# Kernel optimization log

Hardware: AMD Instinct MI355X
Metric: run time of the kernel (lower is better)

## Reference

```python
import jax, jax.numpy as jnp
import numpy as np

B, T, F, E, NH, DH = 32, 256, 224, 32, 4, 64
D = F + E            # block input/output width (n_features + embed_dim) = 256
H = NH * DH          # hidden width = 256
NDYADS = 10000

def _ln(x, g, b):
    mu = jnp.mean(x, axis=-1, keepdims=True)
    v = jnp.var(x, axis=-1, keepdims=True)
    return (x - mu) * jax.lax.rsqrt(v + 1e-5) * g + b

def _mlstm_layer(x, ln_g, ln_b, Wq, Wk, Wv, Wi, Wf, bi, bf, Wo, Wp):
    # pre-norm residual mLSTM block (xLSTM paper, eqs. 19-27, stabilized)
    xn = _ln(x, ln_g, ln_b)
    q = (xn @ Wq).reshape(B, T, NH, DH)
    k = (xn @ Wk).reshape(B, T, NH, DH) * (DH ** -0.5)
    v = (xn @ Wv).reshape(B, T, NH, DH)
    o = jax.nn.sigmoid((xn @ Wo).reshape(B, T, NH, DH))
    ip = xn @ Wi + bi   # [B,T,NH] scalar input-gate preact per head
    fp = xn @ Wf + bf   # [B,T,NH] scalar forget-gate preact per head (exp gate)

    def step(carry, inp):
        C, n, m = carry  # C:[B,NH,DH,DH] matrix memory, n:[B,NH,DH], m:[B,NH]
        qt, kt, vt, ot, it, ft = inp
        m_new = jnp.maximum(ft + m, it)
        i_s = jnp.exp(it - m_new)
        f_s = jnp.exp(ft + m - m_new)
        C = f_s[:, :, None, None] * C + i_s[:, :, None, None] * (vt[:, :, :, None] * kt[:, :, None, :])
        n = f_s[:, :, None] * n + i_s[:, :, None] * kt
        num = jnp.einsum('bhde,bhe->bhd', C, qt)
        den = jnp.maximum(jnp.abs(jnp.einsum('bhd,bhd->bh', n, qt)), 1.0)
        h = ot * num / den[:, :, None]
        return (C, n, m_new), h

    init = (jnp.zeros((B, NH, DH, DH), x.dtype),
            jnp.zeros((B, NH, DH), x.dtype),
            jnp.zeros((B, NH), x.dtype))
    xs = tuple(jnp.moveaxis(a, 1, 0) for a in (q, k, v, o, ip, fp))
    _, hs = jax.lax.scan(step, init, xs)
    h = jnp.moveaxis(hs, 0, 1).reshape(B, T, H)
    return x + h @ Wp

def _slstm_layer(x, ln_g, ln_b, Wz, Wi, Wf, Wo, Rz, Ri, Rf, Ro, Wp):
    # pre-norm residual sLSTM block: exp gating, per-head block-diagonal recurrence
    xn = _ln(x, ln_g, ln_b)
    zx = (xn @ Wz).reshape(B, T, NH, DH)
    ix = (xn @ Wi).reshape(B, T, NH, DH)
    fx = (xn @ Wf).reshape(B, T, NH, DH)
    ox = (xn @ Wo).reshape(B, T, NH, DH)
    rmat = lambda h, R: jnp.einsum('bhd,hde->bhe', h, R)

    def step(carry, inp):
        h, c, n, m = carry  # all [B,NH,DH]
        zt, it, ft, ot = inp
        z = jnp.tanh(zt + rmat(h, Rz))
        ip = it + rmat(h, Ri)
        fp = ft + rmat(h, Rf)
        o = jax.nn.sigmoid(ot + rmat(h, Ro))
        m_new = jnp.maximum(fp + m, ip)
        i_s = jnp.exp(ip - m_new)
        f_s = jnp.exp(fp + m - m_new)
        c = f_s * c + i_s * z
        n = f_s * n + i_s
        h = o * c / n
        return (h, c, n, m_new), h

    z0 = jnp.zeros((B, NH, DH), x.dtype)
    xs = tuple(jnp.moveaxis(a, 1, 0) for a in (zx, ix, fx, ox))
    _, hs = jax.lax.scan(step, (z0, z0, z0, z0), xs)
    h = jnp.moveaxis(hs, 0, 1).reshape(B, T, H)
    return x + h @ Wp

def _forward(X, dyad_idx, embed, mp, sp, fc_W, fc_b):
    emb = embed[dyad_idx]                                              # [B,E]
    x = jnp.concatenate([X, jnp.broadcast_to(emb[:, None, :], (B, T, E))], axis=-1)
    # dropout is identity in eval mode
    x = _mlstm_layer(x, *[p[0] for p in mp])   # layer 'm'
    x = _slstm_layer(x, *sp)                   # layer 's'
    x = _mlstm_layer(x, *[p[1] for p in mp])   # layer 'm'
    return x[:, -1, :] @ fc_W + fc_b           # [B, horizon]

def setup_inputs():
    key = jax.random.key(0)
    ks = jax.random.split(key, 24)
    g = lambda i, shape, s=0.02: jax.random.normal(ks[i], shape, jnp.float32) * s
    return {
        'X': jax.random.normal(ks[0], (B, T, F), jnp.float32),
        'dyad_idx': jax.random.randint(ks[1], (B,), 0, NDYADS),
        'embed': g(2, (NDYADS, E), 0.1),
        'm_ln_g': jnp.ones((2, D), jnp.float32),
        'm_ln_b': jnp.zeros((2, D), jnp.float32),
        'm_Wq': g(3, (2, D, H)), 'm_Wk': g(4, (2, D, H)), 'm_Wv': g(5, (2, D, H)),
        'm_Wi': g(6, (2, D, NH)), 'm_Wf': g(7, (2, D, NH)),
        'm_bi': jnp.zeros((2, NH), jnp.float32),
        'm_bf': jnp.ones((2, NH), jnp.float32),
        'm_Wo': g(8, (2, D, H)), 'm_Wp': g(9, (2, H, D)),
        's_ln_g': jnp.ones((D,), jnp.float32),
        's_ln_b': jnp.zeros((D,), jnp.float32),
        's_Wz': g(10, (D, H)), 's_Wi': g(11, (D, H)), 's_Wf': g(12, (D, H)), 's_Wo': g(13, (D, H)),
        's_Rz': g(14, (NH, DH, DH)), 's_Ri': g(15, (NH, DH, DH)),
        's_Rf': g(16, (NH, DH, DH)), 's_Ro': g(17, (NH, DH, DH)),
        's_Wp': g(18, (H, D)),
        'fc_W': g(19, (D, 1)),
        'fc_b': jnp.zeros((1,), jnp.float32),
    }

def reference(X, dyad_idx, embed, m_ln_g, m_ln_b, m_Wq, m_Wk, m_Wv, m_Wi, m_Wf, m_bi, m_bf, m_Wo, m_Wp, s_ln_g, s_ln_b, s_Wz, s_Wi, s_Wf, s_Wo, s_Rz, s_Ri, s_Rf, s_Ro, s_Wp, fc_W, fc_b):
    mp = (m_ln_g, m_ln_b, m_Wq, m_Wk, m_Wv, m_Wi, m_Wf, m_bi, m_bf, m_Wo, m_Wp)
    sp = (s_ln_g, s_ln_b, s_Wz, s_Wi, s_Wf, s_Wo, s_Rz, s_Ri, s_Rf, s_Ro, s_Wp)
    return _forward(X, dyad_idx, embed, mp, sp, fc_W, fc_b)
```

## Files before the change

kernel.cpp:

```cpp
#include <hip/hip_runtime.h>
#include <hip/hip_bf16.h>


#define BT 8192
#define SZ ((size_t)BT * 256)

typedef __attribute__((ext_vector_type(4))) float  f32x4;
typedef __attribute__((ext_vector_type(8))) short  s16x8;

__device__ __forceinline__ float bf2f(unsigned short u) {
    return __uint_as_float(((unsigned int)u) << 16);
}
__device__ __forceinline__ unsigned short f2bf(float f) {
    __hip_bfloat16 h = __float2bfloat16(f);
    return *(unsigned short*)&h;
}
__device__ __forceinline__ float rdlane(float v, int l) {
    return __int_as_float(__builtin_amdgcn_readlane(__float_as_int(v), l));
}

__global__ __launch_bounds__(256) void conv_w(
    const float* mWq, const float* mWk, const float* mWv, const float* mWo,
    const float* mWp, const float* sWz, const float* sWi, const float* sWf,
    const float* sWo, const float* sWp, unsigned short* __restrict__ Wt)
{
    int z = blockIdx.z;
    const float* mp[5] = {mWq, mWk, mWv, mWo, mWp};
    const float* sp[5] = {sWz, sWi, sWf, sWo, sWp};
    const float* src;
    if (z < 5)       src = mp[z];
    else if (z < 10) src = sp[z - 5];
    else             src = mp[z - 10] + 65536;
    int kB = blockIdx.x * 64, nB = blockIdx.y * 64;
    __shared__ unsigned short Ts[64][68];
    int tid = threadIdx.x;
    int r = tid >> 2, c = (tid & 3) * 16;
    #pragma unroll
    for (int j = 0; j < 16; j += 4) {
        float4 wv = *(const float4*)(src + (size_t)(kB + r) * 256 + nB + c + j);
        Ts[r][c + j]     = f2bf(wv.x); Ts[r][c + j + 1] = f2bf(wv.y);
        Ts[r][c + j + 2] = f2bf(wv.z); Ts[r][c + j + 3] = f2bf(wv.w);
    }
    __syncthreads();
    int n = tid >> 2, k0 = (tid & 3) * 16;
    __attribute__((aligned(16))) unsigned short tmp[16];
    #pragma unroll
    for (int j = 0; j < 16; ++j) tmp[j] = Ts[k0 + j][n];
    unsigned short* dst = Wt + (size_t)z * 65536 + (size_t)(nB + n) * 256 + kB + k0;
    *(uint4*)dst       = *(const uint4*)tmp;
    *(uint4*)(dst + 8) = *(const uint4*)(tmp + 8);
}

__global__ __launch_bounds__(256) void build_x(
    const float* __restrict__ X, const int* __restrict__ dyad,
    const float* __restrict__ embed, float* __restrict__ x)
{
    int i = blockIdx.x * 256 + threadIdx.x;
    int d = i & 255, bt = i >> 8, b = bt >> 8;
    x[i] = (d < 224) ? X[bt * 224 + d] : embed[dyad[b] * 32 + (d - 224)];
}

__global__ __launch_bounds__(256) void layernorm(
    const float* __restrict__ x, const float* __restrict__ g,
    const float* __restrict__ b, unsigned short* __restrict__ xn)
{
    int row = blockIdx.x, tid = threadIdx.x;
    float v = x[(size_t)row * 256 + tid];
    float s = v, s2 = v * v;
    #pragma unroll
    for (int o = 32; o; o >>= 1) { s += __shfl_xor(s, o); s2 += __shfl_xor(s2, o); }
    __shared__ float ls[8];
    int wave = tid >> 6, lane = tid & 63;
    if (lane == 0) { ls[wave] = s; ls[4 + wave] = s2; }
    __syncthreads();
    s  = ls[0] + ls[1] + ls[2] + ls[3];
    s2 = ls[4] + ls[5] + ls[6] + ls[7];
    float mu  = s * (1.f / 256.f);
    float var = s2 * (1.f / 256.f) - mu * mu;
    float inv = rsqrtf(var + 1e-5f);
    xn[(size_t)row * 256 + tid] = f2bf((v - mu) * inv * g[tid] + b[tid]);
}

__global__ __launch_bounds__(256) void gemm_mfma_bf16(
    const unsigned short* __restrict__ A, const unsigned short* __restrict__ Wt,
    int slot0, unsigned short* out0, float a0, float a1, float a2, float a3)
{
    __shared__ unsigned short As[64 * 40];
    __shared__ unsigned short Bs[64 * 40];
    int tid = threadIdx.x, bz = blockIdx.z;
    const unsigned short* W = Wt + (size_t)(slot0 + bz) * 65536;
    unsigned short* out = out0 + (size_t)bz * SZ;
    float alpha = bz == 0 ? a0 : bz == 1 ? a1 : bz == 2 ? a2 : a3;
    int rowBase = blockIdx.x * 64, colBase = blockIdx.y * 64;
    int srow = tid >> 2, scol = (tid & 3) * 8;
    const unsigned short* Ap = A + (size_t)(rowBase + srow) * 256 + scol;
    const unsigned short* Wp = W + (size_t)(colBase + srow) * 256 + scol;
    unsigned short* Asw = As + srow * 40 + scol;
    unsigned short* Bsw = Bs + srow * 40 + scol;
    int w = tid >> 6, lane = tid & 63, quad = lane >> 4, l15 = lane & 15;
    const unsigned short* Ar  = As + (w * 16 + l15) * 40 + quad * 8;
    const unsigned short* Br0 = Bs + l15 * 40 + quad * 8;
    f32x4 acc[4];
    #pragma unroll
    for (int c = 0; c < 4; ++c) acc[c] = (f32x4){0.f, 0.f, 0.f, 0.f};
    for (int k0 = 0; k0 < 256; k0 += 32) {
        uint4 av = *(const uint4*)(Ap + k0);
        uint4 bv = *(const uint4*)(Wp + k0);
        __syncthreads();
        *(uint4*)Asw = av;
        *(uint4*)Bsw = bv;
        __syncthreads();
        s16x8 af = *(const s16x8*)Ar;
        #pragma unroll
        for (int c = 0; c < 4; ++c) {
            s16x8 bf = *(const s16x8*)(Br0 + c * 16 * 40);
            acc[c] = __builtin_amdgcn_mfma_f32_16x16x32_bf16(af, bf, acc[c], 0, 0, 0);
        }
    }
    #pragma unroll
    for (int c = 0; c < 4; ++c) {
        int col  = colBase + c * 16 + l15;
        int row0 = rowBase + w * 16 + quad * 4;
        #pragma unroll
        for (int i2 = 0; i2 < 4; ++i2)
            out[(size_t)(row0 + i2) * 256 + col] = f2bf(alpha * acc[c][i2]);
    }
}

__global__ __launch_bounds__(256) void gemm_mfma_f32(
    const unsigned short* __restrict__ A, const unsigned short* __restrict__ Wt,
    int slot, float* __restrict__ out, const float* __restrict__ Res)
{
    __shared__ unsigned short As[64 * 40];
    __shared__ unsigned short Bs[64 * 40];
    int tid = threadIdx.x;
    const unsigned short* W = Wt + (size_t)slot * 65536;
    int rowBase = blockIdx.x * 64, colBase = blockIdx.y * 64;
    int srow = tid >> 2, scol = (tid & 3) * 8;
    const unsigned short* Ap = A + (size_t)(rowBase + srow) * 256 + scol;
    const unsigned short* Wp = W + (size_t)(colBase + srow) * 256 + scol;
    unsigned short* Asw = As + srow * 40 + scol;
    unsigned short* Bsw = Bs + srow * 40 + scol;
    int w = tid >> 6, lane = tid & 63, quad = lane >> 4, l15 = lane & 15;
    const unsigned short* Ar  = As + (w * 16 + l15) * 40 + quad * 8;
    const unsigned short* Br0 = Bs + l15 * 40 + quad * 8;
    f32x4 acc[4];
    #pragma unroll
    for (int c = 0; c < 4; ++c) acc[c] = (f32x4){0.f, 0.f, 0.f, 0.f};
    for (int k0 = 0; k0 < 256; k0 += 32) {
        uint4 av = *(const uint4*)(Ap + k0);
        uint4 bv = *(const uint4*)(Wp + k0);
        __syncthreads();
        *(uint4*)Asw = av;
        *(uint4*)Bsw = bv;
        __syncthreads();
        s16x8 af = *(const s16x8*)Ar;
        #pragma unroll
        for (int c = 0; c < 4; ++c) {
            s16x8 bf = *(const s16x8*)(Br0 + c * 16 * 40);
            acc[c] = __builtin_amdgcn_mfma_f32_16x16x32_bf16(af, bf, acc[c], 0, 0, 0);
        }
    }
    #pragma unroll
    for (int c = 0; c < 4; ++c) {
        int col  = colBase + c * 16 + l15;
        int row0 = rowBase + w * 16 + quad * 4;
        #pragma unroll
        for (int i2 = 0; i2 < 4; ++i2) {
            size_t idx = (size_t)(row0 + i2) * 256 + col;
            out[idx] = acc[c][i2] + Res[idx];
        }
    }
}

__global__ __launch_bounds__(256) void gate_gemm(
    const unsigned short* __restrict__ xn,
    const float* __restrict__ Wi, const float* __restrict__ Wf,
    const float* __restrict__ bi, const float* __restrict__ bf_,
    float* __restrict__ gi, float* __restrict__ gf)
{
    int tid = threadIdx.x;
    int hh = tid & 3;
    int row = blockIdx.x * 64 + (tid >> 2);
    float ai = bi[hh], af = bf_[hh];
    const unsigned short* xr = xn + (size_t)row * 256;
    for (int k2 = 0; k2 < 256; ++k2) {
        float xv = bf2f(xr[k2]);
        ai += xv * Wi[k2 * 4 + hh];
        af += xv * Wf[k2 * 4 + hh];
    }
    gi[row * 4 + hh] = ai;
    gf[row * 4 + hh] = af;
}

__global__ __launch_bounds__(256) void scan_am(
    const float* __restrict__ gi, const float* __restrict__ gf,
    float* __restrict__ a_arr, float* __restrict__ M_arr)
{
    int bh = blockIdx.x, b = bh >> 2, h = bh & 3;
    int t = threadIdx.x;
    float fp = gf[(b * 256 + t) * 4 + h];
    float ip = gi[(b * 256 + t) * 4 + h];
    __shared__ float buf[256];
    buf[t] = fp;
    __syncthreads();
    #pragma unroll
    for (int o = 1; o < 256; o <<= 1) {
        float add = (t >= o) ? buf[t - o] : 0.f;
        __syncthreads();
        buf[t] += add;
        __syncthreads();
    }
    float F = buf[t];
    float a = ip - F;
    __syncthreads();
    buf[t] = a;
    __syncthreads();
    #pragma unroll
    for (int o = 1; o < 256; o <<= 1) {
        float mx = (t >= o) ? buf[t - o] : -3.4e38f;
        __syncthreads();
        buf[t] = fmaxf(buf[t], mx);
        __syncthreads();
    }
    a_arr[bh * 256 + t] = a;
    M_arr[bh * 256 + t] = fmaxf(buf[t], 0.f);
}

__global__ __launch_bounds__(256) void mlstm_attn(
    const unsigned short* __restrict__ qb, const unsigned short* __restrict__ kb,
    const unsigned short* __restrict__ vb, const unsigned short* __restrict__ ob,
    const float* __restrict__ a_arr, const float* __restrict__ M_arr,
    unsigned short* __restrict__ hout)
{
    int bh = blockIdx.x, rt = blockIdx.y;
    int b = bh >> 2, h = bh & 3;
    int tid = threadIdx.x, w = tid >> 6, lane = tid & 63;
    int quad = lane >> 4, l15 = lane & 15;
    __shared__ unsigned short Qs[64][72];
    __shared__ unsigned short Ks[64][72];
    __shared__ unsigned short Vt[64][72];
    __shared__ unsigned short Ps[4][16][72];
    __shared__ float a_s[64], M_s[64];
    int sr = tid >> 2, sc = (tid & 3) * 16;
    size_t qoff = (size_t)(b * 256 + rt * 64 + sr) * 256 + h * 64 + sc;
    *(uint4*)&Qs[sr][sc]     = *(const uint4*)(qb + qoff);
    *(uint4*)&Qs[sr][sc + 8] = *(const uint4*)(qb + qoff + 8);
    if (tid < 64) M_s[tid] = M_arr[bh * 256 + rt * 64 + tid];
    f32x4 accN[4];
    #pragma unroll
    for (int c = 0; c < 4; ++c) accN[c] = (f32x4){0.f, 0.f, 0.f, 0.f};
    f32x4 den = (f32x4){0.f, 0.f, 0.f, 0.f};
    int rowT = w * 16 + quad * 4;
    for (int ct = 0; ct <= rt; ++ct) {
        size_t koff = (size_t)(b * 256 + ct * 64 + sr) * 256 + h * 64 + sc;
        uint4 kv0 = *(const uint4*)(kb + koff);
        uint4 kv1 = *(const uint4*)(kb + koff + 8);
        uint4 vv0 = *(const uint4*)(vb + koff);
        uint4 vv1 = *(const uint4*)(vb + koff + 8);
        *(uint4*)&Ks[sr][sc]     = kv0;
        *(uint4*)&Ks[sr][sc + 8] = kv1;
        __attribute__((aligned(16))) unsigned short vt[16];
        *(uint4*)vt = vv0; *(uint4*)(vt + 8) = vv1;
        #pragma unroll
        for (int jj = 0; jj < 16; ++jj) Vt[sc + jj][sr] = vt[jj];
        if (tid < 64) a_s[tid] = a_arr[bh * 256 + ct * 64 + tid];
        __syncthreads();
        f32x4 S[4];
        #pragma unroll
        for (int c = 0; c < 4; ++c) S[c] = (f32x4){0.f, 0.f, 0.f, 0.f};
        #pragma unroll
        for (int ks = 0; ks < 2; ++ks) {
            s16x8 af = *(const s16x8*)&Qs[w * 16 + l15][quad * 8 + ks * 32];
            #pragma unroll
            for (int c = 0; c < 4; ++c) {
                s16x8 bfr = *(const s16x8*)&Ks[c * 16 + l15][quad * 8 + ks * 32];
                S[c] = __builtin_amdgcn_mfma_f32_16x16x32_bf16(af, bfr, S[c], 0, 0, 0);
            }
        }
        bool dg = (ct == rt);
        #pragma unroll
        for (int c = 0; c < 4; ++c) {
            int col = c * 16 + l15;
            #pragma unroll
            for (int i2 = 0; i2 < 4; ++i2) {
                int row = rowT + i2;
                float p = S[c][i2] * __expf(a_s[col] - M_s[row]);
                if (dg && col > row) p = 0.f;
                S[c][i2] = p;
                den[i2] += p;
            }
        }
        #pragma unroll
        for (int c = 0; c < 4; ++c)
            #pragma unroll
            for (int i2 = 0; i2 < 4; ++i2)
                Ps[w][quad * 4 + i2][c * 16 + l15] = f2bf(S[c][i2]);
        __syncthreads();
        #pragma unroll
        for (int ks = 0; ks < 2; ++ks) {
            s16x8 af = *(const s16x8*)&Ps[w][l15][quad * 8 + ks * 32];
            #pragma unroll
            for (int c = 0; c < 4; ++c) {
                s16x8 bfr = *(const s16x8*)&Vt[c * 16 + l15][quad * 8 + ks * 32];
                accN[c] = __builtin_amdgcn_mfma_f32_16x16x32_bf16(af, bfr, accN[c], 0, 0, 0);
            }
        }
        __syncthreads();
    }
    #pragma unroll
    for (int ofs = 1; ofs < 16; ofs <<= 1) {
        den[0] += __shfl_xor(den[0], ofs);
        den[1] += __shfl_xor(den[1], ofs);
        den[2] += __shfl_xor(den[2], ofs);
        den[3] += __shfl_xor(den[3], ofs);
    }
    #pragma unroll
    for (int c = 0; c < 4; ++c) {
        int d = c * 16 + l15;
        #pragma unroll
        for (int i2 = 0; i2 < 4; ++i2) {
            size_t idx = (size_t)(b * 256 + rt * 64 + rowT + i2) * 256 + h * 64 + d;
            float ov = bf2f(ob[idx]);
            float sg = 1.f / (1.f + __expf(-ov));
            float dn = fmaxf(fabsf(den[i2]), 1.f);
            hout[idx] = f2bf(sg * accN[c][i2] / dn);
        }
    }
}

__global__ __launch_bounds__(256) void slstm_scan(
    const unsigned short* __restrict__ zx, const unsigned short* __restrict__ ix,
    const unsigned short* __restrict__ fx, const unsigned short* __restrict__ ox,
    const float* __restrict__ Rz, const float* __restrict__ Ri,
    const float* __restrict__ Rf, const float* __restrict__ Ro,
    unsigned short* __restrict__ hout)
{
    int bh = blockIdx.x, b = bh >> 2, h = bh & 3;
    int tid = threadIdx.x, w = tid >> 6, e = tid & 63;
    const float* R = (w == 0 ? Rz : w == 1 ? Ri : w == 2 ? Rf : Ro) + h * 4096;
    float r[64];
    #pragma unroll
    for (int d = 0; d < 64; ++d) r[d] = R[d * 64 + e];
    const unsigned short* xin = (w == 0 ? zx : w == 1 ? ix : w == 2 ? fx : ox);
    __shared__ float gl[2][4][64];
    float c = 0.f, n = 0.f, m = 0.f, hv = 0.f;
    size_t base = (size_t)b * 65536 + h * 64 + e;
    float gx = bf2f(xin[base]);
    for (int t = 0; t < 256; ++t) {
        float a0 = 0.f, a1 = 0.f, a2 = 0.f, a3 = 0.f;
        #pragma unroll
        for (int d = 0; d < 64; d += 4) {
            a0 += rdlane(hv, d)     * r[d];
            a1 += rdlane(hv, d + 1) * r[d + 1];
            a2 += rdlane(hv, d + 2) * r[d + 2];
            a3 += rdlane(hv, d + 3) * r[d + 3];
        }
        gl[t & 1][w][e] = gx + ((a0 + a1) + (a2 + a3));
        int tn = (t + 1 < 256) ? t + 1 : t;
        float gxn = bf2f(xin[base + (size_t)tn * 256]);
        __syncthreads();
        float zp = gl[t & 1][0][e], ip = gl[t & 1][1][e];
        float fp = gl[t & 1][2][e], op = gl[t & 1][3][e];
        float ez = __expf(2.f * zp);
        float z  = 1.f - 2.f / (ez + 1.f);
        float mn = fmaxf(fp + m, ip);
        float i_s = __expf(ip - mn), f_s = __expf(fp + m - mn);
        m = mn;
        c = f_s * c + i_s * z;
        n = f_s * n + i_s;
        hv = (1.f / (1.f + __expf(-op))) * c / n;
        if (w == 0) hout[base + (size_t)t * 256] = f2bf(hv);
        gx = gxn;
    }
}

__global__ __launch_bounds__(64) void fc_kernel(
    const float* __restrict__ x, const float* __restrict__ fcW,
    const float* __restrict__ fcb, float* __restrict__ out)
{
    int b = blockIdx.x, lane = threadIdx.x;
    const float* xr = x + ((size_t)b * 256 + 255) * 256;
    float s = 0.f;
    #pragma unroll
    for (int j = 0; j < 4; ++j) { int d = j * 64 + lane; s += xr[d] * fcW[d]; }
    #pragma unroll
    for (int ofs = 32; ofs; ofs >>= 1) s += __shfl_xor(s, ofs);
    if (lane == 0) out[b] = s + fcb[0];
}

extern "C" void kernel_launch(void* const* d_in, const int* in_sizes, int n_in,
                              void* d_out, int out_size, void* d_ws, size_t ws_size,
                              hipStream_t stream)
{
    const float* X      = (const float*)d_in[0];
    const int*   dyad   = (const int*)d_in[1];
    const float* embed  = (const float*)d_in[2];
    const float* m_ln_g = (const float*)d_in[3];
    const float* m_ln_b = (const float*)d_in[4];
    const float* m_Wq   = (const float*)d_in[5];
    const float* m_Wk   = (const float*)d_in[6];
    const float* m_Wv   = (const float*)d_in[7];
    const float* m_Wi   = (const float*)d_in[8];
    const float* m_Wf   = (const float*)d_in[9];
    const float* m_bi   = (const float*)d_in[10];
    const float* m_bf   = (const float*)d_in[11];
    const float* m_Wo   = (const float*)d_in[12];
    const float* m_Wp   = (const float*)d_in[13];
    const float* s_ln_g = (const float*)d_in[14];
    const float* s_ln_b = (const float*)d_in[15];
    const float* s_Wz   = (const float*)d_in[16];
    const float* s_Wi   = (const float*)d_in[17];
    const float* s_Wf   = (const float*)d_in[18];
    const float* s_Wo   = (const float*)d_in[19];
    const float* s_Rz   = (const float*)d_in[20];
    const float* s_Ri   = (const float*)d_in[21];
    const float* s_Rf   = (const float*)d_in[22];
    const float* s_Ro   = (const float*)d_in[23];
    const float* s_Wp   = (const float*)d_in[24];
    const float* fcW    = (const float*)d_in[25];
    const float* fcb    = (const float*)d_in[26];

    float* ws = (float*)d_ws;
    float* x     = ws;
    float* gi    = x + SZ;
    float* gf    = gi + (size_t)BT * 4;
    float* a_arr = gf + (size_t)BT * 4;
    float* M_arr = a_arr + 32768;
    unsigned short* xn  = (unsigned short*)(M_arr + 32768);
    unsigned short* hb  = xn + SZ;
    unsigned short* g0u = hb + SZ;
    unsigned short* g1u = g0u + SZ;
    unsigned short* g2u = g1u + SZ;
    unsigned short* g3u = g2u + SZ;
    unsigned short* Wt  = g3u + SZ;

    conv_w<<<dim3(4, 4, 15), 256, 0, stream>>>(m_Wq, m_Wk, m_Wv, m_Wo, m_Wp,
                                               s_Wz, s_Wi, s_Wf, s_Wo, s_Wp, Wt);
    build_x<<<8192, 256, 0, stream>>>(X, dyad, embed, x);

    dim3 gg(128, 4);

    auto mlstm = [&](int L) {
        layernorm<<<BT, 256, 0, stream>>>(x, m_ln_g + L * 256, m_ln_b + L * 256, xn);
        gemm_mfma_bf16<<<dim3(128, 4, 4), 256, 0, stream>>>(
            xn, Wt, L * 10, g0u, 1.f, 0.125f, 1.f, 1.f);
        gate_gemm<<<BT / 64, 256, 0, stream>>>(xn, m_Wi + L * 1024, m_Wf + L * 1024,
                                               m_bi + L * 4, m_bf + L * 4, gi, gf);
        scan_am<<<128, 256, 0, stream>>>(gi, gf, a_arr, M_arr);
        mlstm_attn<<<gg, 256, 0, stream>>>(g0u, g1u, g2u, g3u, a_arr, M_arr, hb);
        gemm_mfma_f32<<<dim3(128, 4, 1), 256, 0, stream>>>(hb, Wt, L * 10 + 4, x, x);
    };

    mlstm(0);

    layernorm<<<BT, 256, 0, stream>>>(x, s_ln_g, s_ln_b, xn);
    gemm_mfma_bf16<<<dim3(128, 4, 4), 256, 0, stream>>>(
        xn, Wt, 5, g0u, 1.f, 1.f, 1.f, 1.f);
    slstm_scan<<<128, 256, 0, stream>>>(g0u, g1u, g2u, g3u,
                                        s_Rz, s_Ri, s_Rf, s_Ro, hb);
    gemm_mfma_f32<<<dim3(128, 4, 1), 256, 0, stream>>>(hb, Wt, 9, x, x);

    mlstm(1);

    fc_kernel<<<32, 64, 0, stream>>>(x, fcW, fcb, (float*)d_out);
}
```

Before: 370.7 us.

## Run sLSTM recurrence in a single wave using packed fp16 FMAs

The sLSTM scan kernel shrinks from four waves (one per gate) that synchronise through shared memory every timestep to a single 64-lane wave that computes all four gate recurrences itself. The recurrent weights are held as packed half2 registers, and the hidden-state broadcast uses readlane on a packed pair of values. This removes the per-step __syncthreads and LDS round trip and halves the number of FMA instructions. The cost is fp16 accumulation in the recurrent matvec, which risks precision drift over 256 steps, and each wave now does four times the gate work.

```diff
diff --git a/kernel.cpp b/kernel.cpp
--- a/kernel.cpp
+++ b/kernel.cpp
@@ -1,5 +1,6 @@
 #include <hip/hip_runtime.h>
 #include <hip/hip_bf16.h>
+#include <hip/hip_fp16.h>
 
 
 #define BT 8192
@@ -14,9 +15,6 @@
 __device__ __forceinline__ unsigned short f2bf(float f) {
     __hip_bfloat16 h = __float2bfloat16(f);
     return *(unsigned short*)&h;
-}
-__device__ __forceinline__ float rdlane(float v, int l) {
-    return __int_as_float(__builtin_amdgcn_readlane(__float_as_int(v), l));
 }
 
 __global__ __launch_bounds__(256) void conv_w(
@@ -329,7 +327,7 @@
     }
 }
 
-__global__ __launch_bounds__(256) void slstm_scan(
+__global__ __launch_bounds__(64) void slstm_scan(
     const unsigned short* __restrict__ zx, const unsigned short* __restrict__ ix,
     const unsigned short* __restrict__ fx, const unsigned short* __restrict__ ox,
     const float* __restrict__ Rz, const float* __restrict__ Ri,
@@ -337,41 +335,61 @@
     unsigned short* __restrict__ hout)
 {
     int bh = blockIdx.x, b = bh >> 2, h = bh & 3;
-    int tid = threadIdx.x, w = tid >> 6, e = tid & 63;
-    const float* R = (w == 0 ? Rz : w == 1 ? Ri : w == 2 ? Rf : Ro) + h * 4096;
-    float r[64];
-    #pragma unroll
-    for (int d = 0; d < 64; ++d) r[d] = R[d * 64 + e];
-    const unsigned short* xin = (w == 0 ? zx : w == 1 ? ix : w == 2 ? fx : ox);
-    __shared__ float gl[2][4][64];
+    int e = threadIdx.x;
+    const float* R0 = Rz + h * 4096;
+    const float* R1 = Ri + h * 4096;
+    const float* R2 = Rf + h * 4096;
+    const float* R3 = Ro + h * 4096;
+    __half2 rp0[32], rp1[32], rp2[32], rp3[32];
+    #pragma unroll
+    for (int j = 0; j < 32; ++j) {
+        int o0 = (2 * j) * 64 + e, o1 = (2 * j + 1) * 64 + e;
+        rp0[j] = __floats2half2_rn(R0[o0], R0[o1]);
+        rp1[j] = __floats2half2_rn(R1[o0], R1[o1]);
+        rp2[j] = __floats2half2_rn(R2[o0], R2[o1]);
+        rp3[j] = __floats2half2_rn(R3[o0], R3[o1]);
+    }
     float c = 0.f, n = 0.f, m = 0.f, hv = 0.f;
-    size_t base = (size_t)b * 65536 + h * 64 + e;
-    float gx = bf2f(xin[base]);
+    size_t base = (size_t)(b * 256) * 256 + (size_t)(h * 64 + e);
+    float zv = bf2f(zx[base]), iv = bf2f(ix[base]);
+    float fv = bf2f(fx[base]), ov = bf2f(ox[base]);
+    const __half2 Z2 = __float2half2_rn(0.f);
     for (int t = 0; t < 256; ++t) {
-        float a0 = 0.f, a1 = 0.f, a2 = 0.f, a3 = 0.f;
-        #pragma unroll
-        for (int d = 0; d < 64; d += 4) {
-            a0 += rdlane(hv, d)     * r[d];
-            a1 += rdlane(hv, d + 1) * r[d + 1];
-            a2 += rdlane(hv, d + 2) * r[d + 2];
-            a3 += rdlane(hv, d + 3) * r[d + 3];
-        }
-        gl[t & 1][w][e] = gx + ((a0 + a1) + (a2 + a3));
+        float hn = __shfl_xor(hv, 1);
+        __half2 hp = __floats2half2_rn(hv, hn);
+        union { __half2 h2; unsigned int u; } cv; cv.h2 = hp;
+        unsigned int hbits = cv.u;
+        __half2 A00 = Z2, A01 = Z2, A10 = Z2, A11 = Z2;
+        __half2 A20 = Z2, A21 = Z2, A30 = Z2, A31 = Z2;
+        #pragma unroll
+        for (int j = 0; j < 32; j += 2) {
+            union { unsigned int u; __half2 h2; } c0, c1;
+            c0.u = (unsigned int)__builtin_amdgcn_readlane((int)hbits, 2 * j);
+            c1.u = (unsigned int)__builtin_amdgcn_readlane((int)hbits, 2 * j + 2);
+            A00 = __hfma2(c0.h2, rp0[j], A00);  A01 = __hfma2(c1.h2, rp0[j + 1], A01);
+            A10 = __hfma2(c0.h2, rp1[j], A10);  A11 = __hfma2(c1.h2, rp1[j + 1], A11);
+            A20 = __hfma2(c0.h2, rp2[j], A20);  A21 = __hfma2(c1.h2, rp2[j + 1], A21);
+            A30 = __hfma2(c0.h2, rp3[j], A30);  A31 = __hfma2(c1.h2, rp3[j + 1], A31);
+        }
+        __half2 Az = __hadd2(A00, A01), Ai = __hadd2(A10, A11);
+        __half2 Af = __hadd2(A20, A21), Ao = __hadd2(A30, A31);
+        float zp  = zv + __low2float(Az) + __high2float(Az);
+        float ip2 = iv + __low2float(Ai) + __high2float(Ai);
+        float fp  = fv + __low2float(Af) + __high2float(Af);
+        float op  = ov + __low2float(Ao) + __high2float(Ao);
         int tn = (t + 1 < 256) ? t + 1 : t;
-        float gxn = bf2f(xin[base + (size_t)tn * 256]);
-        __syncthreads();
-        float zp = gl[t & 1][0][e], ip = gl[t & 1][1][e];
-        float fp = gl[t & 1][2][e], op = gl[t & 1][3][e];
+        size_t nb = base + (size_t)tn * 256;
+        zv = bf2f(zx[nb]); iv = bf2f(ix[nb]);
+        fv = bf2f(fx[nb]); ov = bf2f(ox[nb]);
         float ez = __expf(2.f * zp);
         float z  = 1.f - 2.f / (ez + 1.f);
-        float mn = fmaxf(fp + m, ip);
-        float i_s = __expf(ip - mn), f_s = __expf(fp + m - mn);
+        float mn = fmaxf(fp + m, ip2);
+        float i_s = __expf(ip2 - mn), f_s = __expf(fp + m - mn);
         m = mn;
         c = f_s * c + i_s * z;
         n = f_s * n + i_s;
-        hv = (1.f / (1.f + __expf(-op))) * c / n;
-        if (w == 0) hout[base + (size_t)t * 256] = f2bf(hv);
-        gx = gxn;
+        hv = c / (n * (1.f + __expf(-op)));
+        hout[base + (size_t)t * 256] = f2bf(hv);
     }
 }
 
@@ -457,8 +475,8 @@
     layernorm<<<BT, 256, 0, stream>>>(x, s_ln_g, s_ln_b, xn);
     gemm_mfma_bf16<<<dim3(128, 4, 4), 256, 0, stream>>>(
         xn, Wt, 5, g0u, 1.f, 1.f, 1.f, 1.f);
-    slstm_scan<<<128, 256, 0, stream>>>(g0u, g1u, g2u, g3u,
-                                        s_Rz, s_Ri, s_Rf, s_Ro, hb);
+    slstm_scan<<<128, 64, 0, stream>>>(g0u, g1u, g2u, g3u,
+                                       s_Rz, s_Ri, s_Rf, s_Ro, hb);
     gemm_mfma_f32<<<dim3(128, 4, 1), 256, 0, stream>>>(hb, Wt, 9, x, x);
 
     mlstm(1);
```

Measured after the change: 412.6 us. +11.3%, slower.

## Batch sLSTM recurrence across all batches per head using MFMA

Applied to the files above, without the earlier changes.

The sLSTM scan moves from one block per (batch, head) to one block per head that handles all 32 batch rows. Each timestep's recurrent matvec becomes a bf16 MFMA GEMM over [32x64]x[64x64] for the four gates, with h exchanged through double-buffered shared memory. This removes the serial readlane dot products but drops parallelism to only 4 blocks. It also rounds h and the R matrices to bf16 inside the recurrence, which can introduce numerical drift.

```diff
diff --git a/kernel.cpp b/kernel.cpp
--- a/kernel.cpp
+++ b/kernel.cpp
@@ -1,5 +1,6 @@
 #include <hip/hip_runtime.h>
 #include <hip/hip_bf16.h>
+#include <hip/hip_fp16.h>
 
 
 #define BT 8192
@@ -14,9 +15,6 @@
 __device__ __forceinline__ unsigned short f2bf(float f) {
     __hip_bfloat16 h = __float2bfloat16(f);
     return *(unsigned short*)&h;
-}
-__device__ __forceinline__ float rdlane(float v, int l) {
-    return __int_as_float(__builtin_amdgcn_readlane(__float_as_int(v), l));
 }
 
 __global__ __launch_bounds__(256) void conv_w(
@@ -329,49 +327,105 @@
     }
 }
 
-__global__ __launch_bounds__(256) void slstm_scan(
+__global__ __launch_bounds__(512) void slstm_scan(
     const unsigned short* __restrict__ zx, const unsigned short* __restrict__ ix,
     const unsigned short* __restrict__ fx, const unsigned short* __restrict__ ox,
     const float* __restrict__ Rz, const float* __restrict__ Ri,
     const float* __restrict__ Rf, const float* __restrict__ Ro,
     unsigned short* __restrict__ hout)
 {
-    int bh = blockIdx.x, b = bh >> 2, h = bh & 3;
-    int tid = threadIdx.x, w = tid >> 6, e = tid & 63;
-    const float* R = (w == 0 ? Rz : w == 1 ? Ri : w == 2 ? Rf : Ro) + h * 4096;
-    float r[64];
-    #pragma unroll
-    for (int d = 0; d < 64; ++d) r[d] = R[d * 64 + e];
-    const unsigned short* xin = (w == 0 ? zx : w == 1 ? ix : w == 2 ? fx : ox);
-    __shared__ float gl[2][4][64];
-    float c = 0.f, n = 0.f, m = 0.f, hv = 0.f;
-    size_t base = (size_t)b * 65536 + h * 64 + e;
-    float gx = bf2f(xin[base]);
+    int hd = blockIdx.x;
+    int tid = threadIdx.x, w = tid >> 6, lane = tid & 63;
+    int mt = w >> 2, nt = w & 3, quad = lane >> 4, l15 = lane & 15;
+    __shared__ unsigned short hbuf[2][32][72];
+
+    const float* Rg0 = Rz + hd * 4096;
+    const float* Rg1 = Ri + hd * 4096;
+    const float* Rg2 = Rf + hd * 4096;
+    const float* Rg3 = Ro + hd * 4096;
+    int ecol = nt * 16 + l15;
+    s16x8 bfrag[4][2];
+    #pragma unroll
+    for (int ks = 0; ks < 2; ++ks) {
+        int dbase = ks * 32 + quad * 8;
+        #pragma unroll
+        for (int j = 0; j < 8; ++j) {
+            int off = (dbase + j) * 64 + ecol;
+            bfrag[0][ks][j] = (short)f2bf(Rg0[off]);
+            bfrag[1][ks][j] = (short)f2bf(Rg1[off]);
+            bfrag[2][ks][j] = (short)f2bf(Rg2[off]);
+            bfrag[3][ks][j] = (short)f2bf(Rg3[off]);
+        }
+    }
+    for (int i = tid; i < 2 * 32 * 72; i += 512)
+        ((unsigned short*)hbuf)[i] = 0;
+
+    int b0 = mt * 16 + quad * 4;
+    const unsigned short* xg0 = zx; const unsigned short* xg1 = ix;
+    const unsigned short* xg2 = fx; const unsigned short* xg3 = ox;
+    size_t xbase[4];
+    #pragma unroll
+    for (int r = 0; r < 4; ++r)
+        xbase[r] = (size_t)(b0 + r) * 65536 + hd * 64 + ecol;
+
+    unsigned short xc[4][4];
+    #pragma unroll
+    for (int r = 0; r < 4; ++r) {
+        xc[0][r] = xg0[xbase[r]]; xc[1][r] = xg1[xbase[r]];
+        xc[2][r] = xg2[xbase[r]]; xc[3][r] = xg3[xbase[r]];
+    }
+    float cst[4] = {0.f, 0.f, 0.f, 0.f};
+    float nst[4] = {0.f, 0.f, 0.f, 0.f};
+    float mst[4] = {0.f, 0.f, 0.f, 0.f};
+    __syncthreads();
+
+    int cur = 0;
+    int arow = mt * 16 + l15;
     for (int t = 0; t < 256; ++t) {
-        float a0 = 0.f, a1 = 0.f, a2 = 0.f, a3 = 0.f;
-        #pragma unroll
-        for (int d = 0; d < 64; d += 4) {
-            a0 += rdlane(hv, d)     * r[d];
-            a1 += rdlane(hv, d + 1) * r[d + 1];
-            a2 += rdlane(hv, d + 2) * r[d + 2];
-            a3 += rdlane(hv, d + 3) * r[d + 3];
-        }
-        gl[t & 1][w][e] = gx + ((a0 + a1) + (a2 + a3));
-        int tn = (t + 1 < 256) ? t + 1 : t;
-        float gxn = bf2f(xin[base + (size_t)tn * 256]);
-        __syncthreads();
-        float zp = gl[t & 1][0][e], ip = gl[t & 1][1][e];
-        float fp = gl[t & 1][2][e], op = gl[t & 1][3][e];
-        float ez = __expf(2.f * zp);
-        float z  = 1.f - 2.f / (ez + 1.f);
-        float mn = fmaxf(fp + m, ip);
-        float i_s = __expf(ip - mn), f_s = __expf(fp + m - mn);
-        m = mn;
-        c = f_s * c + i_s * z;
-        n = f_s * n + i_s;
-        hv = (1.f / (1.f + __expf(-op))) * c / n;
-        if (w == 0) hout[base + (size_t)t * 256] = f2bf(hv);
-        gx = gxn;
+        unsigned short xnx[4][4];
+        size_t toff = (size_t)((t + 1 < 256) ? t + 1 : t) * 256;
+        #pragma unroll
+        for (int r = 0; r < 4; ++r) {
+            xnx[0][r] = xg0[xbase[r] + toff]; xnx[1][r] = xg1[xbase[r] + toff];
+            xnx[2][r] = xg2[xbase[r] + toff]; xnx[3][r] = xg3[xbase[r] + toff];
+        }
+        s16x8 af0 = *(const s16x8*)&hbuf[cur][arow][quad * 8];
+        s16x8 af1 = *(const s16x8*)&hbuf[cur][arow][32 + quad * 8];
+        f32x4 acc[4];
+        #pragma unroll
+        for (int g = 0; g < 4; ++g)
+            acc[g] = (f32x4){bf2f(xc[g][0]), bf2f(xc[g][1]),
+                             bf2f(xc[g][2]), bf2f(xc[g][3])};
+        #pragma unroll
+        for (int g = 0; g < 4; ++g) {
+            acc[g] = __builtin_amdgcn_mfma_f32_16x16x32_bf16(af0, bfrag[g][0], acc[g], 0, 0, 0);
+            acc[g] = __builtin_amdgcn_mfma_f32_16x16x32_bf16(af1, bfrag[g][1], acc[g], 0, 0, 0);
+        }
+        size_t tstore = (size_t)t * 256;
+        #pragma unroll
+        for (int r = 0; r < 4; ++r) {
+            float zp = acc[0][r], ip2 = acc[1][r];
+            float fp = acc[2][r], op  = acc[3][r];
+            float ez = __expf(2.f * zp);
+            float z  = 1.f - 2.f / (ez + 1.f);
+            float fpm = fp + mst[r];
+            float mn = fmaxf(fpm, ip2);
+            float i_s = __expf(ip2 - mn), f_s = __expf(fpm - mn);
+            mst[r] = mn;
+            cst[r] = f_s * cst[r] + i_s * z;
+            nst[r] = f_s * nst[r] + i_s;
+            float hv = cst[r] / (nst[r] * (1.f + __expf(-op)));
+            unsigned short hb16 = f2bf(hv);
+            hbuf[cur ^ 1][b0 + r][ecol] = hb16;
+            hout[xbase[r] + tstore] = hb16;
+        }
+        #pragma unroll
+        for (int r = 0; r < 4; ++r) {
+            xc[0][r] = xnx[0][r]; xc[1][r] = xnx[1][r];
+            xc[2][r] = xnx[2][r]; xc[3][r] = xnx[3][r];
+        }
+        __syncthreads();
+        cur ^= 1;
     }
 }
 
@@ -457,8 +511,8 @@
     layernorm<<<BT, 256, 0, stream>>>(x, s_ln_g, s_ln_b, xn);
     gemm_mfma_bf16<<<dim3(128, 4, 4), 256, 0, stream>>>(
         xn, Wt, 5, g0u, 1.f, 1.f, 1.f, 1.f);
-    slstm_scan<<<128, 256, 0, stream>>>(g0u, g1u, g2u, g3u,
-                                        s_Rz, s_Ri, s_Rf, s_Ro, hb);
+    slstm_scan<<<4, 512, 0, stream>>>(g0u, g1u, g2u, g3u,
+                                      s_Rz, s_Ri, s_Rf, s_Ro, hb);
     gemm_mfma_f32<<<dim3(128, 4, 1), 256, 0, stream>>>(hb, Wt, 9, x, x);
 
     mlstm(1);
```

After: 529.1 us. 42.7% more time.
